# Kernel optimization log

Hardware: AMD Instinct MI355X
Metric: run time of the kernel (lower is better)

The kernel has to match this reference:

```python
import jax, jax.numpy as jnp
import numpy as np

NUM_NODES = 50000
NUM_EDGES = 800000
DIM = 64
NUM_REL2 = 400
NUM_LAYERS = 3
NUM_TAILS = 512


def setup_inputs() -> dict:
    key = jax.random.key(0)
    ks = jax.random.split(key, 16)
    s = lambda shape, k, scale: jax.random.normal(k, shape, jnp.float32) * scale
    return {
        'head_embeds': s((DIM,), ks[0], 1.0),
        'rel_table': s((NUM_REL2, DIM), ks[1], 0.1),
        'rel_W': s((NUM_LAYERS, NUM_REL2, DIM), ks[2], 0.1),
        'agg_W': s((NUM_LAYERS, 8 * DIM, DIM), ks[3], (8 * DIM) ** -0.5),
        'agg_b': jnp.zeros((NUM_LAYERS, DIM), jnp.float32),
        'lin_W': s((2 * DIM, DIM), ks[4], (2 * DIM) ** -0.5),
        'lin_b': jnp.zeros((DIM,), jnp.float32),
        'mlp_W1': s((DIM, 2 * DIM), ks[5], DIM ** -0.5),
        'mlp_b1': jnp.zeros((2 * DIM,), jnp.float32),
        'mlp_W2': s((2 * DIM, 1), ks[6], (2 * DIM) ** -0.5),
        'mlp_b2': jnp.zeros((1,), jnp.float32),
        'edge_src': jax.random.randint(ks[7], (NUM_EDGES,), 0, NUM_NODES, jnp.int32),
        'edge_dst': jax.random.randint(ks[8], (NUM_EDGES,), 0, NUM_NODES, jnp.int32),
        'edge_type': jax.random.randint(ks[9], (NUM_EDGES,), 0, NUM_REL2, jnp.int32),
        'head_index': 0,
        'r_index': 7,
        't_index': jax.random.randint(ks[10], (NUM_TAILS,), 0, NUM_NODES, jnp.int32),
    }


def _score_fn(hidden, query, lin_W, lin_b, mlp_W1, mlp_b1, mlp_W2, mlp_b2):
    # hidden: [N, d], query: [d]
    q = jnp.broadcast_to(query, hidden.shape)
    heuristic = jnp.concatenate([hidden, q], axis=-1) @ lin_W + lin_b  # [N, d]
    x = hidden * heuristic
    h1 = jax.nn.relu(x @ mlp_W1 + mlp_b1)
    return (h1 @ mlp_W2 + mlp_b2)[..., 0]  # [N]


def reference(head_embeds, rel_table, rel_W, agg_W, agg_b, lin_W, lin_b,
              mlp_W1, mlp_b1, mlp_W2, mlp_b2,
              edge_src, edge_dst, edge_type, head_index, r_index, t_index):
    N, d = NUM_NODES, DIM
    score_fn = lambda h, q: _score_fn(h, q, lin_W, lin_b, mlp_W1, mlp_b1, mlp_W2, mlp_b2)

    query = rel_table[r_index]  # [d]

    # init_input_embeds: boundary zeros except head node; init score
    hidden = jnp.zeros((N, d), jnp.float32).at[head_index].set(head_embeds)
    zero_s = score_fn(jnp.zeros((1, d), jnp.float32), query)[0]
    score = jnp.full((N,), zero_s, jnp.float32)
    score = score.at[head_index].set(score_fn(head_embeds[None, :], query)[0])
    score = jnp.clip(score, -15.0, 15.0)

    deg = jax.ops.segment_sum(jnp.ones_like(edge_dst, jnp.float32), edge_dst, N)  # [N]
    deg_safe = jnp.maximum(deg, 1.0)
    has_in = deg > 0
    pna_degree_mean = jnp.log(deg + 1.0).mean()
    scale = (jnp.log(deg + 1.0) / pna_degree_mean)[:, None]  # [N,1]

    for l in range(NUM_LAYERS):
        gate = jax.nn.sigmoid(score)[:, None]  # [N,1]
        layer_input = gate * hidden  # [N,d]
        # relational messages: gather + per-relation transform
        msg = layer_input[edge_src] * rel_W[l][edge_type]  # [E,d]
        # PNA aggregators per destination node
        ssum = jax.ops.segment_sum(msg, edge_dst, N)
        mean = ssum / deg_safe[:, None]
        sq = jax.ops.segment_sum(msg * msg, edge_dst, N) / deg_safe[:, None]
        std = jnp.sqrt(jnp.maximum(sq - mean * mean, 0.0) + 1e-6)
        mx = jax.ops.segment_max(msg, edge_dst, N)
        mn = jax.ops.segment_min(msg, edge_dst, N)
        mx = jnp.where(has_in[:, None], mx, 0.0)
        mn = jnp.where(has_in[:, None], mn, 0.0)
        feat = jnp.concatenate([mean, mx, mn, std], axis=-1)  # [N,4d]
        feat = jnp.concatenate([feat, feat * scale], axis=-1)  # [N,8d]
        update = feat @ agg_W[l] + agg_b[l]  # [N,d]
        # residual update only for nodes with incoming edges
        hidden = hidden + jnp.where(has_in[:, None], update, 0.0)
        new_score = score_fn(hidden, query)
        score = jnp.where(has_in, new_score, score)

    return score[t_index]  # [NUM_TAILS]
```

## Files before the change

kernel.cpp:

```cpp
#include <hip/hip_runtime.h>
#include <math.h>

#define NN 50000
#define NREL 400
#define NLAYERS 3

static __device__ __forceinline__ float clip15(float x) { return fminf(fmaxf(x, -15.f), 15.f); }

__global__ void count_k(const int* __restrict__ dst, int* __restrict__ deg, int E) {
  int e = blockIdx.x * blockDim.x + threadIdx.x;
  if (e < E) atomicAdd(&deg[dst[e]], 1);
}

__global__ void scan_k(const int* __restrict__ deg, int* __restrict__ start, int* __restrict__ cursor,
                       int* __restrict__ counter, float* __restrict__ logsum, int N) {
  int n = blockIdx.x * blockDim.x + threadIdx.x;
  int lane = threadIdx.x & 63;
  int d = (n < N) ? deg[n] : 0;
  int pre = d;
  #pragma unroll
  for (int off = 1; off < 64; off <<= 1) { int t = __shfl_up(pre, off); if (lane >= off) pre += t; }
  int base = 0;
  if (lane == 63) base = atomicAdd(counter, pre);
  base = __shfl(base, 63);
  if (n < N) { int pos = base + pre - d; start[n] = pos; cursor[n] = pos; }
  float v = (n < N) ? logf((float)d + 1.0f) : 0.f;
  #pragma unroll
  for (int off = 32; off; off >>= 1) v += __shfl_xor(v, off);
  if (lane == 0) atomicAdd(logsum, v);
}

__global__ void scale_k(const int* __restrict__ deg, const float* __restrict__ logsum,
                        float* __restrict__ scale, int N) {
  int n = blockIdx.x * blockDim.x + threadIdx.x;
  if (n < N) scale[n] = logf((float)deg[n] + 1.0f) * (float)N / logsum[0];
}

__global__ void scatter_k(const int* __restrict__ src, const int* __restrict__ dst,
                          const int* __restrict__ typ, int* __restrict__ cursor,
                          int2* __restrict__ csr, int E) {
  int e = blockIdx.x * blockDim.x + threadIdx.x;
  if (e < E) {
    int dd = dst[e];
    int pos = atomicAdd(&cursor[dd], 1);
    csr[pos] = make_int2(src[e], typ[e]);
  }
}

__global__ void prep_k(const float* __restrict__ head_embeds, const float* __restrict__ rel_table,
                       const float* __restrict__ lin_W, const float* __restrict__ lin_b,
                       const float* __restrict__ mlp_W1, const float* __restrict__ mlp_b1,
                       const float* __restrict__ mlp_W2, const float* __restrict__ mlp_b2,
                       const int* __restrict__ head_index, const int* __restrict__ r_index,
                       float* __restrict__ hidden, float* __restrict__ scalars) {
  int j = threadIdx.x;
  int r = r_index[0], hd = head_index[0];
  float qj = rel_table[r * 64 + j];
  float cq = lin_b[j];
  for (int k = 0; k < 64; ++k) cq += __shfl(qj, k) * lin_W[(64 + k) * 64 + j];
  scalars[j] = cq;
  float t = fmaxf(mlp_b1[j], 0.f) * mlp_W2[j] + fmaxf(mlp_b1[64 + j], 0.f) * mlp_W2[64 + j];
  #pragma unroll
  for (int off = 32; off; off >>= 1) t += __shfl_xor(t, off);
  float zs = clip15(t + mlp_b2[0]);
  float hj = head_embeds[j];
  hidden[(size_t)hd * 64 + j] = hj;
  float heur = cq;
  for (int k = 0; k < 64; ++k) heur += __shfl(hj, k) * lin_W[k * 64 + j];
  float xj = hj * heur;
  float h1a = mlp_b1[j], h1b = mlp_b1[64 + j];
  for (int k = 0; k < 64; ++k) {
    float xk = __shfl(xj, k);
    h1a += xk * mlp_W1[k * 128 + j];
    h1b += xk * mlp_W1[k * 128 + 64 + j];
  }
  h1a = fmaxf(h1a, 0.f); h1b = fmaxf(h1b, 0.f);
  float p = h1a * mlp_W2[j] + h1b * mlp_W2[64 + j];
  #pragma unroll
  for (int off = 32; off; off >>= 1) p += __shfl_xor(p, off);
  float hs = clip15(p + mlp_b2[0]);
  if (j == 0) { scalars[64] = zs; scalars[65] = hs; }
}

__global__ void fill_k(float* __restrict__ score, const float* __restrict__ scalars,
                       const int* __restrict__ head_index, int N) {
  int n = blockIdx.x * blockDim.x + threadIdx.x;
  if (n < N) score[n] = (n == head_index[0]) ? scalars[65] : scalars[64];
}

__global__ void gate_k(const float* __restrict__ hidden, const float* __restrict__ score,
                       float* __restrict__ LI, int N) {
  int i = blockIdx.x * blockDim.x + threadIdx.x;
  if (i < N * 16) {
    int node = i >> 4;
    float s = score[node];
    float g = 1.f / (1.f + expf(-s));
    float4 h = ((const float4*)hidden)[i];
    float4 r = make_float4(h.x * g, h.y * g, h.z * g, h.w * g);
    ((float4*)LI)[i] = r;
  }
}

__global__ __launch_bounds__(256) void agg_k(const float* __restrict__ LI, const int2* __restrict__ csr,
                                             const int* __restrict__ start, const int* __restrict__ deg,
                                             const float* __restrict__ relW, float* __restrict__ f1, int N) {
  int wid = threadIdx.x >> 6;
  int lane = threadIdx.x & 63;
  int node = blockIdx.x * 4 + wid;
  if (node >= N) return;
  int base = start[node], d = deg[node];
  float sum = 0.f, sq = 0.f, mx = -3.402823e38f, mn = 3.402823e38f;
  int e = 0;
  for (; e + 4 <= d; e += 4) {
    int2 p0 = csr[base + e], p1 = csr[base + e + 1];
    int2 p2 = csr[base + e + 2], p3 = csr[base + e + 3];
    float a0 = LI[p0.x * 64 + lane], w0 = relW[p0.y * 64 + lane];
    float a1 = LI[p1.x * 64 + lane], w1 = relW[p1.y * 64 + lane];
    float a2 = LI[p2.x * 64 + lane], w2 = relW[p2.y * 64 + lane];
    float a3 = LI[p3.x * 64 + lane], w3 = relW[p3.y * 64 + lane];
    float m0 = a0 * w0, m1 = a1 * w1, m2 = a2 * w2, m3 = a3 * w3;
    sum += (m0 + m1) + (m2 + m3);
    sq += (m0 * m0 + m1 * m1) + (m2 * m2 + m3 * m3);
    mx = fmaxf(fmaxf(mx, fmaxf(m0, m1)), fmaxf(m2, m3));
    mn = fminf(fminf(mn, fminf(m0, m1)), fminf(m2, m3));
  }
  for (; e < d; ++e) {
    int2 p = csr[base + e];
    float m = LI[p.x * 64 + lane] * relW[p.y * 64 + lane];
    sum += m; sq += m * m; mx = fmaxf(mx, m); mn = fminf(mn, m);
  }
  float* out = f1 + (size_t)node * 256;
  if (d > 0) {
    float inv = 1.0f / (float)d;
    float mean = sum * inv, sqm = sq * inv;
    float sd = sqrtf(fmaxf(sqm - mean * mean, 0.f) + 1e-6f);
    out[lane] = mean; out[64 + lane] = mx; out[128 + lane] = mn; out[192 + lane] = sd;
  } else {
    out[lane] = 0.f; out[64 + lane] = 0.f; out[128 + lane] = 0.f; out[192 + lane] = 0.f;
  }
}

__global__ __launch_bounds__(512) void gemm_k(const float* __restrict__ f1, const float* __restrict__ aggW,
                                              const float* __restrict__ aggb, const float* __restrict__ scale,
                                              const int* __restrict__ deg, float* __restrict__ hidden, int N) {
  __shared__ float At[32][66];
  __shared__ float Was[32][64];
  __shared__ float Wbs[32][64];
  int tid = threadIdx.x;
  int tx = tid & 15;
  int tn = tid >> 4;
  int n0 = blockIdx.x * 64;
  float acc_a[2][4] = {{0.f}}, acc_b[2][4] = {{0.f}};
  int anode = tid >> 3;
  int ak = (tid & 7) * 4;
  bool avalid = (n0 + anode) < N;
  const float* Arow = f1 + (size_t)(n0 + anode) * 256 + ak;
  const float4* WaG = (const float4*)(aggW);
  const float4* WbG = (const float4*)(aggW + (size_t)256 * 64);

  for (int kc = 0; kc < 8; ++kc) {
    float4 v = make_float4(0.f, 0.f, 0.f, 0.f);
    if (avalid) v = *(const float4*)(Arow + kc * 32);
    At[ak + 0][anode] = v.x; At[ak + 1][anode] = v.y;
    At[ak + 2][anode] = v.z; At[ak + 3][anode] = v.w;
    ((float4*)Was)[tid] = WaG[kc * 512 + tid];
    ((float4*)Wbs)[tid] = WbG[kc * 512 + tid];
    __syncthreads();
    #pragma unroll 8
    for (int kk = 0; kk < 32; ++kk) {
      float2 a  = *(const float2*)&At[kk][tn * 2];
      float4 wa = *(const float4*)&Was[kk][tx * 4];
      float4 wb = *(const float4*)&Wbs[kk][tx * 4];
      acc_a[0][0] += a.x * wa.x; acc_a[0][1] += a.x * wa.y; acc_a[0][2] += a.x * wa.z; acc_a[0][3] += a.x * wa.w;
      acc_a[1][0] += a.y * wa.x; acc_a[1][1] += a.y * wa.y; acc_a[1][2] += a.y * wa.z; acc_a[1][3] += a.y * wa.w;
      acc_b[0][0] += a.x * wb.x; acc_b[0][1] += a.x * wb.y; acc_b[0][2] += a.x * wb.z; acc_b[0][3] += a.x * wb.w;
      acc_b[1][0] += a.y * wb.x; acc_b[1][1] += a.y * wb.y; acc_b[1][2] += a.y * wb.z; acc_b[1][3] += a.y * wb.w;
    }
    __syncthreads();
  }

  float4 bj = *(const float4*)(aggb + tx * 4);
  #pragma unroll
  for (int i = 0; i < 2; ++i) {
    int node = n0 + tn * 2 + i;
    if (node < N && deg[node] > 0) {
      float sc = scale[node];
      float4* hp = (float4*)(hidden + (size_t)node * 64 + tx * 4);
      float4 h = *hp;
      h.x += acc_a[i][0] + sc * acc_b[i][0] + bj.x;
      h.y += acc_a[i][1] + sc * acc_b[i][1] + bj.y;
      h.z += acc_a[i][2] + sc * acc_b[i][2] + bj.z;
      h.w += acc_a[i][3] + sc * acc_b[i][3] + bj.w;
      *hp = h;
    }
  }
}

#define SC_LDS 12992
__global__ __launch_bounds__(256) void score2_k(const float* __restrict__ hidden, float* __restrict__ score,
                                                const int* __restrict__ deg, const float* __restrict__ lin_W,
                                                const float* __restrict__ mlp_W1, const float* __restrict__ mlp_b1,
                                                const float* __restrict__ mlp_W2, const float* __restrict__ mlp_b2,
                                                const float* __restrict__ scalars, int N) {
  __shared__ float smem[SC_LDS];
  float* X   = smem;
  float* H   = smem + 4160;
  float* WA  = smem + 8320;
  float* W1s = smem + 4160;
  float* sW2 = smem + 12416;
  float* sb1 = smem + 12544;
  float* scq = smem + 12672;
  float* pred= smem + 12736;

  int t = threadIdx.x;
  int lane = t & 63;
  int g = t >> 6;
  int n0 = blockIdx.x * 64;

  for (int i = t; i < 1024; i += 256) ((float4*)WA)[i] = ((const float4*)lin_W)[i];
  if (t < 128) { sW2[t] = mlp_W2[t]; sb1[t] = mlp_b1[t]; }
  if (t < 64) scq[t] = scalars[t];
  for (int i = t; i < 1024; i += 256) {
    int node = i >> 4;
    int k4 = (i & 15) << 2;
    float4 v = make_float4(0.f, 0.f, 0.f, 0.f);
    if (n0 + node < N) v = ((const float4*)(hidden + (size_t)(n0 + node) * 64))[i & 15];
    float* hp = &H[node * 65 + k4];
    hp[0] = v.x; hp[1] = v.y; hp[2] = v.z; hp[3] = v.w;
  }
  __syncthreads();

  float acc[16];
  #pragma unroll
  for (int i = 0; i < 16; ++i) acc[i] = scq[g * 16 + i];
  #pragma unroll 8
  for (int kk = 0; kk < 64; ++kk) {
    float h = H[lane * 65 + kk];
    const float4* wr = (const float4*)&WA[kk * 64 + g * 16];
    float4 w0 = wr[0], w1 = wr[1], w2 = wr[2], w3 = wr[3];
    acc[0]  += h * w0.x; acc[1]  += h * w0.y; acc[2]  += h * w0.z; acc[3]  += h * w0.w;
    acc[4]  += h * w1.x; acc[5]  += h * w1.y; acc[6]  += h * w1.z; acc[7]  += h * w1.w;
    acc[8]  += h * w2.x; acc[9]  += h * w2.y; acc[10] += h * w2.z; acc[11] += h * w2.w;
    acc[12] += h * w3.x; acc[13] += h * w3.y; acc[14] += h * w3.z; acc[15] += h * w3.w;
  }
  #pragma unroll
  for (int i = 0; i < 16; ++i) {
    int j = g * 16 + i;
    X[lane * 65 + j] = H[lane * 65 + j] * acc[i];
  }
  __syncthreads();

  for (int i = t; i < 2048; i += 256) ((float4*)W1s)[i] = ((const float4*)mlp_W1)[i];
  __syncthreads();

  float acc2[32];
  #pragma unroll
  for (int i = 0; i < 32; ++i) acc2[i] = sb1[g * 32 + i];
  #pragma unroll 4
  for (int kk = 0; kk < 64; ++kk) {
    float xv = X[lane * 65 + kk];
    const float4* wr = (const float4*)&W1s[kk * 128 + g * 32];
    #pragma unroll
    for (int s = 0; s < 8; ++s) {
      float4 w = wr[s];
      acc2[s * 4 + 0] += xv * w.x; acc2[s * 4 + 1] += xv * w.y;
      acc2[s * 4 + 2] += xv * w.z; acc2[s * 4 + 3] += xv * w.w;
    }
  }
  float p = 0.f;
  #pragma unroll
  for (int i = 0; i < 32; ++i) p += fmaxf(acc2[i], 0.f) * sW2[g * 32 + i];
  pred[g * 64 + lane] = p;
  __syncthreads();
  if (t < 64) {
    int node = n0 + t;
    if (node < N && deg[node] > 0)
      score[node] = pred[t] + pred[64 + t] + pred[128 + t] + pred[192 + t] + mlp_b2[0];
  }
}

__global__ void out_k(const float* __restrict__ score, const int* __restrict__ t_index,
                      float* __restrict__ out, int T) {
  int i = blockIdx.x * blockDim.x + threadIdx.x;
  if (i < T) out[i] = score[t_index[i]];
}

extern "C" void kernel_launch(void* const* d_in, const int* in_sizes, int n_in,
                              void* d_out, int out_size, void* d_ws, size_t ws_size,
                              hipStream_t stream) {
  const float* head_embeds = (const float*)d_in[0];
  const float* rel_table   = (const float*)d_in[1];
  const float* rel_W       = (const float*)d_in[2];
  const float* agg_W       = (const float*)d_in[3];
  const float* agg_b       = (const float*)d_in[4];
  const float* lin_W       = (const float*)d_in[5];
  const float* lin_b       = (const float*)d_in[6];
  const float* mlp_W1      = (const float*)d_in[7];
  const float* mlp_b1      = (const float*)d_in[8];
  const float* mlp_W2      = (const float*)d_in[9];
  const float* mlp_b2      = (const float*)d_in[10];
  const int* edge_src      = (const int*)d_in[11];
  const int* edge_dst      = (const int*)d_in[12];
  const int* edge_type     = (const int*)d_in[13];
  const int* head_index    = (const int*)d_in[14];
  const int* r_index       = (const int*)d_in[15];
  const int* t_index       = (const int*)d_in[16];
  int E = in_sizes[11];
  int T = in_sizes[16];
  int N = NN;

  char* w = (char*)d_ws;
  size_t off = 0;
  auto alloc = [&](size_t bytes) {
    void* p = w + off;
    off = (off + bytes + 255) & ~(size_t)255;
    return p;
  };
  int* deg      = (int*)alloc((size_t)N * 4);
  int* start    = (int*)alloc((size_t)N * 4);
  int* cursor   = (int*)alloc((size_t)N * 4);
  float* scale  = (float*)alloc((size_t)N * 4);
  int* counter  = (int*)alloc(4);
  float* logsum = (float*)alloc(4);
  float* scalars= (float*)alloc(66 * 4);
  int2* csr     = (int2*)alloc((size_t)E * 8);
  float* hidden = (float*)alloc((size_t)N * 64 * 4);
  float* score  = (float*)alloc((size_t)N * 4);
  float* LI     = (float*)alloc((size_t)N * 64 * 4);
  float* f1     = (float*)alloc((size_t)N * 256 * 4);
  if (off > ws_size) return;

  hipMemsetAsync(deg, 0, (size_t)N * 4, stream);
  hipMemsetAsync(counter, 0, 4, stream);
  hipMemsetAsync(logsum, 0, 4, stream);
  hipMemsetAsync(hidden, 0, (size_t)N * 64 * 4, stream);

  count_k<<<(E + 255) / 256, 256, 0, stream>>>(edge_dst, deg, E);
  scan_k<<<(N + 255) / 256, 256, 0, stream>>>(deg, start, cursor, counter, logsum, N);
  scale_k<<<(N + 255) / 256, 256, 0, stream>>>(deg, logsum, scale, N);
  scatter_k<<<(E + 255) / 256, 256, 0, stream>>>(edge_src, edge_dst, edge_type, cursor, csr, E);
  prep_k<<<1, 64, 0, stream>>>(head_embeds, rel_table, lin_W, lin_b, mlp_W1, mlp_b1, mlp_W2, mlp_b2,
                               head_index, r_index, hidden, scalars);
  fill_k<<<(N + 255) / 256, 256, 0, stream>>>(score, scalars, head_index, N);

  for (int l = 0; l < NLAYERS; ++l) {
    gate_k<<<(N * 16 + 255) / 256, 256, 0, stream>>>(hidden, score, LI, N);
    agg_k<<<(N + 3) / 4, 256, 0, stream>>>(LI, csr, start, deg, rel_W + (size_t)l * NREL * 64, f1, N);
    gemm_k<<<(N + 63) / 64, 512, 0, stream>>>(f1, agg_W + (size_t)l * 512 * 64, agg_b + (size_t)l * 64,
                                              scale, deg, hidden, N);
    score2_k<<<(N + 63) / 64, 256, 0, stream>>>(hidden, score, deg, lin_W, mlp_W1, mlp_b1, mlp_W2, mlp_b2,
                                                scalars, N);
  }
  out_k<<<(T + 255) / 256, 256, 0, stream>>>(score, t_index, (float*)d_out, T);
}
```

Baseline: 619.2 us.

## Fuse sigmoid gating into edge aggregation and enlarge GEMM per-thread tile

Removes the separate gate kernel and the LI buffer. The aggregation kernel now reads hidden and score directly and computes the sigmoid gate for each source node on the fly, saving one full read and write pass over the node features per layer. The cost is redundant exp work per edge: every lane recomputes the gate, which is about 16x more sigmoid evaluations than before. Separately, the update GEMM drops from 512 to 128 threads per block, each computing 8 nodes × 8 outputs instead of 2 × 8. This raises register reuse but also register pressure, and cuts parallelism within a block.

```diff
diff --git a/kernel.cpp b/kernel.cpp
--- a/kernel.cpp
+++ b/kernel.cpp
@@ -88,20 +88,8 @@
   if (n < N) score[n] = (n == head_index[0]) ? scalars[65] : scalars[64];
 }
 
-__global__ void gate_k(const float* __restrict__ hidden, const float* __restrict__ score,
-                       float* __restrict__ LI, int N) {
-  int i = blockIdx.x * blockDim.x + threadIdx.x;
-  if (i < N * 16) {
-    int node = i >> 4;
-    float s = score[node];
-    float g = 1.f / (1.f + expf(-s));
-    float4 h = ((const float4*)hidden)[i];
-    float4 r = make_float4(h.x * g, h.y * g, h.z * g, h.w * g);
-    ((float4*)LI)[i] = r;
-  }
-}
-
-__global__ __launch_bounds__(256) void agg_k(const float* __restrict__ LI, const int2* __restrict__ csr,
+__global__ __launch_bounds__(256) void agg_k(const float* __restrict__ hidden, const float* __restrict__ score,
+                                             const int2* __restrict__ csr,
                                              const int* __restrict__ start, const int* __restrict__ deg,
                                              const float* __restrict__ relW, float* __restrict__ f1, int N) {
   int wid = threadIdx.x >> 6;
@@ -114,10 +102,14 @@
   for (; e + 4 <= d; e += 4) {
     int2 p0 = csr[base + e], p1 = csr[base + e + 1];
     int2 p2 = csr[base + e + 2], p3 = csr[base + e + 3];
-    float a0 = LI[p0.x * 64 + lane], w0 = relW[p0.y * 64 + lane];
-    float a1 = LI[p1.x * 64 + lane], w1 = relW[p1.y * 64 + lane];
-    float a2 = LI[p2.x * 64 + lane], w2 = relW[p2.y * 64 + lane];
-    float a3 = LI[p3.x * 64 + lane], w3 = relW[p3.y * 64 + lane];
+    float g0 = 1.f / (1.f + expf(-score[p0.x]));
+    float g1 = 1.f / (1.f + expf(-score[p1.x]));
+    float g2 = 1.f / (1.f + expf(-score[p2.x]));
+    float g3 = 1.f / (1.f + expf(-score[p3.x]));
+    float a0 = g0 * hidden[p0.x * 64 + lane], w0 = relW[p0.y * 64 + lane];
+    float a1 = g1 * hidden[p1.x * 64 + lane], w1 = relW[p1.y * 64 + lane];
+    float a2 = g2 * hidden[p2.x * 64 + lane], w2 = relW[p2.y * 64 + lane];
+    float a3 = g3 * hidden[p3.x * 64 + lane], w3 = relW[p3.y * 64 + lane];
     float m0 = a0 * w0, m1 = a1 * w1, m2 = a2 * w2, m3 = a3 * w3;
     sum += (m0 + m1) + (m2 + m3);
     sq += (m0 * m0 + m1 * m1) + (m2 * m2 + m3 * m3);
@@ -126,7 +118,9 @@
   }
   for (; e < d; ++e) {
     int2 p = csr[base + e];
-    float m = LI[p.x * 64 + lane] * relW[p.y * 64 + lane];
+    float g = 1.f / (1.f + expf(-score[p.x]));
+    float li = g * hidden[p.x * 64 + lane];
+    float m = li * relW[p.y * 64 + lane];
     sum += m; sq += m * m; mx = fmaxf(mx, m); mn = fminf(mn, m);
   }
   float* out = f1 + (size_t)node * 256;
@@ -140,49 +134,67 @@
   }
 }
 
-__global__ __launch_bounds__(512) void gemm_k(const float* __restrict__ f1, const float* __restrict__ aggW,
+__global__ __launch_bounds__(128) void gemm_k(const float* __restrict__ f1, const float* __restrict__ aggW,
                                               const float* __restrict__ aggb, const float* __restrict__ scale,
                                               const int* __restrict__ deg, float* __restrict__ hidden, int N) {
-  __shared__ float At[32][66];
+  __shared__ float At[32][68];
   __shared__ float Was[32][64];
   __shared__ float Wbs[32][64];
   int tid = threadIdx.x;
   int tx = tid & 15;
   int tn = tid >> 4;
   int n0 = blockIdx.x * 64;
-  float acc_a[2][4] = {{0.f}}, acc_b[2][4] = {{0.f}};
-  int anode = tid >> 3;
-  int ak = (tid & 7) * 4;
+  float acc_a[8][4] = {{0.f}}, acc_b[8][4] = {{0.f}};
+  int anode = tid >> 1;
+  int akh = (tid & 1) * 16;
   bool avalid = (n0 + anode) < N;
-  const float* Arow = f1 + (size_t)(n0 + anode) * 256 + ak;
+  const float* Arow = f1 + (size_t)(n0 + anode) * 256 + akh;
   const float4* WaG = (const float4*)(aggW);
   const float4* WbG = (const float4*)(aggW + (size_t)256 * 64);
 
   for (int kc = 0; kc < 8; ++kc) {
-    float4 v = make_float4(0.f, 0.f, 0.f, 0.f);
-    if (avalid) v = *(const float4*)(Arow + kc * 32);
-    At[ak + 0][anode] = v.x; At[ak + 1][anode] = v.y;
-    At[ak + 2][anode] = v.z; At[ak + 3][anode] = v.w;
-    ((float4*)Was)[tid] = WaG[kc * 512 + tid];
-    ((float4*)Wbs)[tid] = WbG[kc * 512 + tid];
+    float4 v[4];
+    if (avalid) {
+      const float4* ap = (const float4*)(Arow + kc * 32);
+      #pragma unroll
+      for (int s = 0; s < 4; ++s) v[s] = ap[s];
+    } else {
+      #pragma unroll
+      for (int s = 0; s < 4; ++s) v[s] = make_float4(0.f, 0.f, 0.f, 0.f);
+    }
+    #pragma unroll
+    for (int s = 0; s < 4; ++s) {
+      At[akh + s * 4 + 0][anode] = v[s].x; At[akh + s * 4 + 1][anode] = v[s].y;
+      At[akh + s * 4 + 2][anode] = v[s].z; At[akh + s * 4 + 3][anode] = v[s].w;
+    }
+    #pragma unroll
+    for (int i = 0; i < 4; ++i) {
+      ((float4*)Was)[tid + i * 128] = WaG[kc * 512 + tid + i * 128];
+      ((float4*)Wbs)[tid + i * 128] = WbG[kc * 512 + tid + i * 128];
+    }
     __syncthreads();
-    #pragma unroll 8
+    #pragma unroll 4
     for (int kk = 0; kk < 32; ++kk) {
-      float2 a  = *(const float2*)&At[kk][tn * 2];
+      float4 a0 = *(const float4*)&At[kk][tn * 8];
+      float4 a1 = *(const float4*)&At[kk][tn * 8 + 4];
       float4 wa = *(const float4*)&Was[kk][tx * 4];
       float4 wb = *(const float4*)&Wbs[kk][tx * 4];
-      acc_a[0][0] += a.x * wa.x; acc_a[0][1] += a.x * wa.y; acc_a[0][2] += a.x * wa.z; acc_a[0][3] += a.x * wa.w;
-      acc_a[1][0] += a.y * wa.x; acc_a[1][1] += a.y * wa.y; acc_a[1][2] += a.y * wa.z; acc_a[1][3] += a.y * wa.w;
-      acc_b[0][0] += a.x * wb.x; acc_b[0][1] += a.x * wb.y; acc_b[0][2] += a.x * wb.z; acc_b[0][3] += a.x * wb.w;
-      acc_b[1][0] += a.y * wb.x; acc_b[1][1] += a.y * wb.y; acc_b[1][2] += a.y * wb.z; acc_b[1][3] += a.y * wb.w;
+      float an[8] = {a0.x, a0.y, a0.z, a0.w, a1.x, a1.y, a1.z, a1.w};
+      #pragma unroll
+      for (int i = 0; i < 8; ++i) {
+        acc_a[i][0] += an[i] * wa.x; acc_a[i][1] += an[i] * wa.y;
+        acc_a[i][2] += an[i] * wa.z; acc_a[i][3] += an[i] * wa.w;
+        acc_b[i][0] += an[i] * wb.x; acc_b[i][1] += an[i] * wb.y;
+        acc_b[i][2] += an[i] * wb.z; acc_b[i][3] += an[i] * wb.w;
+      }
     }
     __syncthreads();
   }
 
   float4 bj = *(const float4*)(aggb + tx * 4);
   #pragma unroll
-  for (int i = 0; i < 2; ++i) {
-    int node = n0 + tn * 2 + i;
+  for (int i = 0; i < 8; ++i) {
+    int node = n0 + tn * 8 + i;
     if (node < N && deg[node] > 0) {
       float sc = scale[node];
       float4* hp = (float4*)(hidden + (size_t)node * 64 + tx * 4);
@@ -326,7 +338,6 @@
   int2* csr     = (int2*)alloc((size_t)E * 8);
   float* hidden = (float*)alloc((size_t)N * 64 * 4);
   float* score  = (float*)alloc((size_t)N * 4);
-  float* LI     = (float*)alloc((size_t)N * 64 * 4);
   float* f1     = (float*)alloc((size_t)N * 256 * 4);
   if (off > ws_size) return;
 
@@ -344,9 +355,9 @@
   fill_k<<<(N + 255) / 256, 256, 0, stream>>>(score, scalars, head_index, N);
 
   for (int l = 0; l < NLAYERS; ++l) {
-    gate_k<<<(N * 16 + 255) / 256, 256, 0, stream>>>(hidden, score, LI, N);
-    agg_k<<<(N + 3) / 4, 256, 0, stream>>>(LI, csr, start, deg, rel_W + (size_t)l * NREL * 64, f1, N);
-    gemm_k<<<(N + 63) / 64, 512, 0, stream>>>(f1, agg_W + (size_t)l * 512 * 64, agg_b + (size_t)l * 64,
+    agg_k<<<(N + 3) / 4, 256, 0, stream>>>(hidden, score, csr, start, deg,
+                                           rel_W + (size_t)l * NREL * 64, f1, N);
+    gemm_k<<<(N + 63) / 64, 128, 0, stream>>>(f1, agg_W + (size_t)l * 512 * 64, agg_b + (size_t)l * 64,
                                               scale, deg, hidden, N);
     score2_k<<<(N + 63) / 64, 256, 0, stream>>>(hidden, score, deg, lin_W, mlp_W1, mlp_b1, mlp_W2, mlp_b2,
                                                 scalars, N);
```

After: 661.3 us. 6.8% more time.
